# Kernel optimization log

Hardware: AMD Instinct MI355X
Metric: run time of the kernel (lower is better)

## Reference

```python
import jax, jax.numpy as jnp
import numpy as np

C = 512

def setup_inputs() -> dict:
    key = jax.random.key(0)
    ks = jax.random.split(key, 7)
    x = jax.random.normal(ks[0], (4, C, 64, 64), dtype=jnp.float32)
    s = 1.0 / np.sqrt(C)
    f_w = jax.random.normal(ks[1], (C // 2, C), dtype=jnp.float32) * s
    f_b = jax.random.normal(ks[2], (C // 2,), dtype=jnp.float32) * 0.01
    g_w = jax.random.normal(ks[3], (C // 2, C), dtype=jnp.float32) * s
    g_b = jax.random.normal(ks[4], (C // 2,), dtype=jnp.float32) * 0.01
    h_w = jax.random.normal(ks[5], (C, C), dtype=jnp.float32) * s
    h_b = jax.random.normal(ks[6], (C,), dtype=jnp.float32) * 0.01
    return {"x": x, "f_w": f_w, "f_b": f_b, "g_w": g_w, "g_b": g_b, "h_w": h_w, "h_b": h_b}

def reference(x, f_w, f_b, g_w, g_b, h_w, h_b):
    B, Cc, H, W = x.shape
    N = H * W
    xf = x.reshape(B, Cc, N)  # hw_flatten
    # 1x1 convs are channel GEMMs: [B,Cout,N]
    f = jnp.einsum('oc,bcn->bon', f_w, xf) + f_b[None, :, None]
    g = jnp.einsum('oc,bcn->bon', g_w, xf) + g_b[None, :, None]
    h = jnp.einsum('oc,bcn->bon', h_w, xf) + h_b[None, :, None]
    # energy[b,i,j] = sum_k f[b,k,i] * g[b,k,j]
    energy = jnp.einsum('bki,bkj->bij', f, g)
    attention = jax.nn.softmax(energy, axis=-1)
    # ret[b,c,i] = sum_j h[b,c,j] * attention[b,i,j]
    ret = jnp.einsum('bcj,bij->bci', h, attention)
    return ret.reshape(B, Cc, H, W)
```

## Files before the change

kernel.cpp:

```cpp
#include <hip/hip_runtime.h>


#define NPIX 4096
#define CIN  512

typedef _Float16 f16x4 __attribute__((ext_vector_type(4)));
typedef _Float16 f16x8 __attribute__((ext_vector_type(8)));
typedef float    f32x4 __attribute__((ext_vector_type(4)));
typedef float    f32x16 __attribute__((ext_vector_type(16)));

#define MFMA16(a, b, c) __builtin_amdgcn_mfma_f32_16x16x16f16(a, b, c, 0, 0, 0)
#define MFMA32(a, b, c) __builtin_amdgcn_mfma_f32_32x32x16_f16(a, b, c, 0, 0, 0)

__device__ __forceinline__ void gld_lds16(const void* g, void* l) {
    __builtin_amdgcn_global_load_lds(
        (const __attribute__((address_space(1))) unsigned int*)g,
        (__attribute__((address_space(3))) unsigned int*)l, 16, 0, 0);
}

__global__ __launch_bounds__(256) void proj_kernel(
    const float* __restrict__ x,
    const float* __restrict__ f_w, const float* __restrict__ f_b,
    const float* __restrict__ g_w, const float* __restrict__ g_b,
    const float* __restrict__ h_w, const float* __restrict__ h_b,
    _Float16* __restrict__ qw, _Float16* __restrict__ kw,
    _Float16* __restrict__ vw)
{
    const int b  = blockIdx.z;
    const int n0 = blockIdx.x * 64;
    const int o0 = blockIdx.y * 64;

    const float* wsrc; const float* bsrc;
    if (o0 < 256)      { wsrc = f_w + (size_t)o0 * CIN;         bsrc = f_b + o0; }
    else if (o0 < 512) { wsrc = g_w + (size_t)(o0 - 256) * CIN; bsrc = g_b + (o0 - 256); }
    else               { wsrc = h_w + (size_t)(o0 - 512) * CIN; bsrc = h_b + (o0 - 512); }

    __shared__ _Float16 Wt[64][40];
    __shared__ _Float16 Xt[64][40];

    const int t = threadIdx.x;
    const int lane = t & 63, wv = t >> 6;
    const int wm = wv >> 1, wn = wv & 1;
    const int gi = lane >> 4, li = lane & 15;

    f32x4 acc[2][2];
    #pragma unroll
    for (int i = 0; i < 2; ++i)
        #pragma unroll
        for (int j = 0; j < 2; ++j) acc[i][j] = f32x4{0.f, 0.f, 0.f, 0.f};

    for (int kk = 0; kk < CIN; kk += 32) {
        {
            const int r = t >> 2, c8 = (t & 3) * 8;
            const float* p = wsrc + (size_t)r * CIN + kk + c8;
            const float4 v0 = *(const float4*)p;
            const float4 v1 = *(const float4*)(p + 4);
            f16x8 w8;
            w8[0] = (_Float16)v0.x; w8[1] = (_Float16)v0.y;
            w8[2] = (_Float16)v0.z; w8[3] = (_Float16)v0.w;
            w8[4] = (_Float16)v1.x; w8[5] = (_Float16)v1.y;
            w8[6] = (_Float16)v1.z; w8[7] = (_Float16)v1.w;
            *(f16x8*)&Wt[r][c8] = w8;
        }
        {
            const int cb = (t >> 6) * 8;
            const int nl = t & 63;
            f16x8 xv;
            #pragma unroll
            for (int e = 0; e < 8; ++e)
                xv[e] = (_Float16)x[((size_t)b * CIN + kk + cb + e) * NPIX +
                                    n0 + nl];
            *(f16x8*)&Xt[nl][cb] = xv;
        }
        __syncthreads();
        #pragma unroll
        for (int kh = 0; kh < 2; ++kh) {
            const int ko = kh * 16 + gi * 4;
            f16x4 a0 = *(const f16x4*)&Wt[wm * 32 +      li][ko];
            f16x4 a1 = *(const f16x4*)&Wt[wm * 32 + 16 + li][ko];
            f16x4 b0 = *(const f16x4*)&Xt[wn * 32 +      li][ko];
            f16x4 b1 = *(const f16x4*)&Xt[wn * 32 + 16 + li][ko];
            acc[0][0] = MFMA16(a0, b0, acc[0][0]);
            acc[0][1] = MFMA16(a0, b1, acc[0][1]);
            acc[1][0] = MFMA16(a1, b0, acc[1][0]);
            acc[1][1] = MFMA16(a1, b1, acc[1][1]);
        }
        __syncthreads();
    }

    #pragma unroll
    for (int mf = 0; mf < 2; ++mf)
        #pragma unroll
        for (int nf = 0; nf < 2; ++nf) {
            const int obase = o0 + wm * 32 + mf * 16 + gi * 4;
            const int n     = n0 + wn * 32 + nf * 16 + li;
            const int brel  = wm * 32 + mf * 16 + gi * 4;
            float v[4];
            #pragma unroll
            for (int r = 0; r < 4; ++r) v[r] = acc[mf][nf][r] + bsrc[brel + r];
            if (o0 < 512) {
                _Float16* dst = (o0 < 256) ? qw : kw;
                const int kb  = (o0 < 256) ? obase : (obase - 256);
                f16x4 pk;
                pk[0] = (_Float16)v[0]; pk[1] = (_Float16)v[1];
                pk[2] = (_Float16)v[2]; pk[3] = (_Float16)v[3];
                *(f16x4*)&dst[((size_t)b * NPIX + n) * 256 + kb] = pk;
            } else {
                #pragma unroll
                for (int r = 0; r < 4; ++r)
                    vw[((size_t)b * CIN + (obase - 512 + r)) * NPIX + n] =
                        (_Float16)v[r];
            }
        }
}

__global__ __launch_bounds__(512, 2) void attn_kernel(
    const _Float16* __restrict__ qw, const _Float16* __restrict__ kw,
    const _Float16* __restrict__ vw,
    _Float16* __restrict__ opart, float* __restrict__ stats)
{
    const int bid = blockIdx.x;
    const int xcd = bid & 7;
    const int jh = xcd & 1, b = xcd >> 1;
    const int rb = bid >> 3;
    const int t = threadIdx.x, l = t & 63, wv = t >> 6;
    const int li = l & 31, g = l >> 5;
    const int ch = wv & 1, rg = wv >> 1;
    const int i_row = rb * 128 + rg * 32 + li;

    __shared__ char Kt[2][16384];
    __shared__ char Vt[2][512 * 72];
    __shared__ char Pt[2][4][64 * 48];

    f16x8 qf[16];
    if (ch == 0) {
        const _Float16* qb = qw + ((size_t)b * NPIX + i_row) * 256 + 8 * g;
        #pragma unroll
        for (int ks = 0; ks < 16; ++ks) qf[ks] = *(const f16x8*)(qb + ks * 16);
    }

    f32x16 oacc[8];
    #pragma unroll
    for (int i = 0; i < 8; ++i)
        #pragma unroll
        for (int e = 0; e < 16; ++e) oacc[i][e] = 0.f;
    float m_run = -__builtin_inff();
    float l_run = 0.f;

    f16x8 vreg[4];

    auto stageK = [&](int buf, int j0) {
        #pragma unroll
        for (int q = 0; q < 2; ++q) {
            const int slot = q * 512 + t;
            const int row  = slot >> 5;
            const int colb = (slot & 31) * 16;
            const char* src =
                (const char*)(kw + ((size_t)b * NPIX + j0 + row) * 256) +
                (colb ^ ((row & 31) << 4));
            gld_lds16(src, Kt[buf] + slot * 16);
        }
    };
    auto loadV = [&](int j0) {
        #pragma unroll
        for (int q = 0; q < 4; ++q) {
            const int c  = q * 128 + (t >> 2);
            const int jj = (t & 3) * 8;
            vreg[q] = *(const f16x8*)(vw + ((size_t)b * CIN + c) * NPIX + j0 + jj);
        }
    };
    auto writeV = [&](int buf) {
        #pragma unroll
        for (int q = 0; q < 4; ++q) {
            const int c = q * 128 + (t >> 2);
            char* d = Vt[buf] + c * 72 + (t & 3) * 16;
            *(f16x4*)d       = *(f16x4*)&vreg[q];
            *(f16x4*)(d + 8) = *((f16x4*)&vreg[q] + 1);
        }
    };

    const int jbase = jh * 2048;
    stageK(0, jbase);
    loadV(jbase);
    writeV(0);
    __syncthreads();

    for (int it = 0; it < 64; ++it) {
        const int cur = it & 1;
        if (it < 63) {
            stageK(cur ^ 1, jbase + (it + 1) * 32);
            loadV(jbase + (it + 1) * 32);
        }

        f16x8 pa0, pa1;
        if (ch == 0) {
            f32x16 s;
            #pragma unroll
            for (int e = 0; e < 16; ++e) s[e] = 0.f;
            {
                const char* kr = Kt[cur] + li * 512;
                const int sw = li << 4;
                __builtin_amdgcn_s_setprio(1);
                #pragma unroll
                for (int ks = 0; ks < 16; ++ks) {
                    f16x8 kf = *(const f16x8*)(kr + ((ks * 32 + 16 * g) ^ sw));
                    s = MFMA32(kf, qf[ks], s);
                }
                __builtin_amdgcn_s_setprio(0);
            }

            float tmax = s[0];
            #pragma unroll
            for (int e = 1; e < 16; ++e) tmax = fmaxf(tmax, s[e]);
            tmax = fmaxf(tmax, __shfl_xor(tmax, 32));
            float sc_my = 1.0f;
            if (!__all((int)(tmax - m_run <= 5.f))) {
                const float mnew = fmaxf(m_run, tmax);
                sc_my = __expf(m_run - mnew);
                #pragma unroll
                for (int ct = 0; ct < 8; ++ct)
                    #pragma unroll
                    for (int e = 0; e < 16; ++e) oacc[ct][e] *= sc_my;
                l_run *= sc_my;
                m_run = mnew;
            }
            float p[16];
            float rs = 0.f;
            #pragma unroll
            for (int e = 0; e < 16; ++e) { p[e] = __expf(s[e] - m_run); rs += p[e]; }
            rs += __shfl_xor(rs, 32);
            l_run += rs;

            #pragma unroll
            for (int e = 0; e < 8; ++e) {
                pa0[e] = (_Float16)p[e];
                pa1[e] = (_Float16)p[8 + e];
            }
            char* pd = Pt[cur][rg] + l * 48;
            *(f16x8*)pd        = pa0;
            *(f16x8*)(pd + 16) = pa1;
            *(float*)(pd + 32) = sc_my;
        }
        __syncthreads();

        if (ch == 1) {
            const char* ps = Pt[cur][rg] + l * 48;
            pa0 = *(const f16x8*)ps;
            pa1 = *(const f16x8*)(ps + 16);
            const float sc = *(const float*)(ps + 32);
            if (!__all((int)(sc == 1.0f))) {
                #pragma unroll
                for (int ct = 0; ct < 8; ++ct)
                    #pragma unroll
                    for (int e = 0; e < 16; ++e) oacc[ct][e] *= sc;
            }
        }

        __builtin_amdgcn_s_setprio(1);
        #pragma unroll
        for (int ct = 0; ct < 8; ++ct) {
            const int c = ch * 256 + ct * 32 + li;
            const char* vr = Vt[cur] + c * 72;
            f16x8 va;
            *(f16x4*)&va       = *(const f16x4*)(vr + 8 * g);
            *((f16x4*)&va + 1) = *(const f16x4*)(vr + 16 + 8 * g);
            oacc[ct] = MFMA32(va, pa0, oacc[ct]);
            f16x8 vc;
            *(f16x4*)&vc       = *(const f16x4*)(vr + 32 + 8 * g);
            *((f16x4*)&vc + 1) = *(const f16x4*)(vr + 48 + 8 * g);
            oacc[ct] = MFMA32(vc, pa1, oacc[ct]);
        }
        __builtin_amdgcn_s_setprio(0);

        if (it < 63) writeV(cur ^ 1);
    }

    const size_t ob = (size_t)(jh * 4 + b) * CIN * NPIX;
    #pragma unroll
    for (int ct = 0; ct < 8; ++ct)
        #pragma unroll
        for (int r = 0; r < 16; ++r) {
            const int c = ch * 256 + ct * 32 + (r & 3) + 8 * (r >> 2) + 4 * g;
            opart[ob + (size_t)c * NPIX + i_row] = (_Float16)oacc[ct][r];
        }
    if (ch == 0 && g == 0) {
        const size_t idx = ((size_t)(jh * 4 + b) * NPIX + i_row) * 2;
        stats[idx]     = m_run;
        stats[idx + 1] = l_run;
    }
}

__global__ __launch_bounds__(256) void combine_kernel(
    const _Float16* __restrict__ opart, const float* __restrict__ stats,
    float* __restrict__ out)
{
    const int b  = blockIdx.y;
    const int i0 = blockIdx.x * 64;
    const int t  = threadIdx.x;

    __shared__ float a0s[64], a1s[64];
    if (t < 64) {
        const int i = i0 + t;
        const size_t r0 = ((size_t)b * NPIX + i) * 2;
        const size_t r1 = ((size_t)(4 + b) * NPIX + i) * 2;
        const float m0 = stats[r0], l0 = stats[r0 + 1];
        const float m1 = stats[r1], l1 = stats[r1 + 1];
        const float M  = fmaxf(m0, m1);
        const float w0 = __expf(m0 - M), w1 = __expf(m1 - M);
        const float inv = 1.0f / (l0 * w0 + l1 * w1);
        a0s[t] = w0 * inv;
        a1s[t] = w1 * inv;
    }
    __syncthreads();

    const int ci = t >> 3;
    const int ii = (t & 7) * 8;
    #pragma unroll 4
    for (int pp = 0; pp < 16; ++pp) {
        const int c = pp * 32 + ci;
        const _Float16* p0 = opart + ((size_t)b * CIN + c) * NPIX + i0 + ii;
        const _Float16* p1 = opart + ((size_t)(4 + b) * CIN + c) * NPIX + i0 + ii;
        const f16x8 x0 = *(const f16x8*)p0;
        const f16x8 x1 = *(const f16x8*)p1;
        float* dst = out + ((size_t)b * CIN + c) * NPIX + i0 + ii;
        float4 o0, o1;
        o0.x = a0s[ii + 0] * (float)x0[0] + a1s[ii + 0] * (float)x1[0];
        o0.y = a0s[ii + 1] * (float)x0[1] + a1s[ii + 1] * (float)x1[1];
        o0.z = a0s[ii + 2] * (float)x0[2] + a1s[ii + 2] * (float)x1[2];
        o0.w = a0s[ii + 3] * (float)x0[3] + a1s[ii + 3] * (float)x1[3];
        o1.x = a0s[ii + 4] * (float)x0[4] + a1s[ii + 4] * (float)x1[4];
        o1.y = a0s[ii + 5] * (float)x0[5] + a1s[ii + 5] * (float)x1[5];
        o1.z = a0s[ii + 6] * (float)x0[6] + a1s[ii + 6] * (float)x1[6];
        o1.w = a0s[ii + 7] * (float)x0[7] + a1s[ii + 7] * (float)x1[7];
        *(float4*)dst       = o0;
        *(float4*)(dst + 4) = o1;
    }
}

extern "C" void kernel_launch(void* const* d_in, const int* in_sizes, int n_in,
                              void* d_out, int out_size, void* d_ws,
                              size_t ws_size, hipStream_t stream)
{
    const float* x   = (const float*)d_in[0];
    const float* f_w = (const float*)d_in[1];
    const float* f_b = (const float*)d_in[2];
    const float* g_w = (const float*)d_in[3];
    const float* g_b = (const float*)d_in[4];
    const float* h_w = (const float*)d_in[5];
    const float* h_b = (const float*)d_in[6];
    float* out = (float*)d_out;

    _Float16* qw = (_Float16*)d_ws;
    _Float16* kw = qw + (size_t)4 * NPIX * 256;
    _Float16* vw = kw + (size_t)4 * NPIX * 256;
    _Float16* op = vw + (size_t)4 * CIN * NPIX;
    float* stats = (float*)(op + (size_t)2 * 4 * CIN * NPIX);

    proj_kernel<<<dim3(64, 16, 4), 256, 0, stream>>>(
        x, f_w, f_b, g_w, g_b, h_w, h_b, qw, kw, vw);
    attn_kernel<<<dim3(256), 512, 0, stream>>>(qw, kw, vw, op, stats);
    combine_kernel<<<dim3(64, 4), 256, 0, stream>>>(op, stats, out);
}
```

Before: 235.8 us.

## Software-pipeline attention so QK of step s overlaps PV of step s-1

Restructures the attention main loop so the score-computing waves (ch==0) run QK^T and softmax for the current key tile, then apply the previous tile's P·V for their share of channels. The other waves meanwhile do P·V for the previous tile. This drops one of the two __syncthreads per iteration, so softmax no longer stalls the PV waves. Channel work is rebalanced 192/320 between the two wave groups to offset the QK cost, and V writes to LDS are moved to the loop start. The trade-off is more accumulator registers (10 tiles) on the PV waves, which may reduce occupancy, plus extra prologue and epilogue code.

```diff
diff --git a/kernel.cpp b/kernel.cpp
--- a/kernel.cpp
+++ b/kernel.cpp
@@ -16,6 +16,31 @@
     __builtin_amdgcn_global_load_lds(
         (const __attribute__((address_space(1))) unsigned int*)g,
         (__attribute__((address_space(3))) unsigned int*)l, 16, 0, 0);
+}
+
+template<int NCT, int CB>
+__device__ __forceinline__ void pv_step(f32x16* oacc, const char* vb,
+                                        int li, int g, f16x8 pa0, f16x8 pa1) {
+    #pragma unroll
+    for (int ct = 0; ct < NCT; ++ct) {
+        const int c = CB + ct * 32 + li;
+        const char* vr = vb + c * 72;
+        f16x8 va, vc;
+        *(f16x4*)&va       = *(const f16x4*)(vr + 8 * g);
+        *((f16x4*)&va + 1) = *(const f16x4*)(vr + 16 + 8 * g);
+        oacc[ct] = MFMA32(va, pa0, oacc[ct]);
+        *(f16x4*)&vc       = *(const f16x4*)(vr + 32 + 8 * g);
+        *((f16x4*)&vc + 1) = *(const f16x4*)(vr + 48 + 8 * g);
+        oacc[ct] = MFMA32(vc, pa1, oacc[ct]);
+    }
+}
+
+template<int N>
+__device__ __forceinline__ void rescale_acc(f32x16* o, float sc) {
+    #pragma unroll
+    for (int ct = 0; ct < N; ++ct)
+        #pragma unroll
+        for (int e = 0; e < 16; ++e) o[ct][e] *= sc;
 }
 
 __global__ __launch_bounds__(256) void proj_kernel(
@@ -125,7 +150,7 @@
     const int rb = bid >> 3;
     const int t = threadIdx.x, l = t & 63, wv = t >> 6;
     const int li = l & 31, g = l >> 5;
-    const int ch = wv & 1, rg = wv >> 1;
+    const int ch = wv >> 2, rg = wv & 3;
     const int i_row = rb * 128 + rg * 32 + li;
 
     __shared__ char Kt[2][16384];
@@ -139,15 +164,19 @@
         for (int ks = 0; ks < 16; ++ks) qf[ks] = *(const f16x8*)(qb + ks * 16);
     }
 
-    f32x16 oacc[8];
-    #pragma unroll
-    for (int i = 0; i < 8; ++i)
+    f32x16 oacc[10];
+    #pragma unroll
+    for (int i = 0; i < 10; ++i)
         #pragma unroll
         for (int e = 0; e < 16; ++e) oacc[i][e] = 0.f;
     float m_run = -__builtin_inff();
     float l_run = 0.f;
 
     f16x8 vreg[4];
+    f16x8 paA, paB;
+    float sc_prev = 1.0f;
+    #pragma unroll
+    for (int e = 0; e < 8; ++e) { paA[e] = (_Float16)0; paB[e] = (_Float16)0; }
 
     auto stageK = [&](int buf, int j0) {
         #pragma unroll
@@ -180,23 +209,28 @@
     };
 
     const int jbase = jh * 2048;
+    loadV(jbase);
     stageK(0, jbase);
-    loadV(jbase);
-    writeV(0);
+    if (ch == 0) {
+        char* pd = Pt[1][rg] + l * 48;
+        *(f16x8*)pd        = paA;
+        *(f16x8*)(pd + 16) = paB;
+        *(float*)(pd + 32) = 1.0f;
+    }
     __syncthreads();
 
-    for (int it = 0; it < 64; ++it) {
-        const int cur = it & 1;
-        if (it < 63) {
-            stageK(cur ^ 1, jbase + (it + 1) * 32);
-            loadV(jbase + (it + 1) * 32);
-        }
-
-        f16x8 pa0, pa1;
+    for (int s = 0; s < 64; ++s) {
+        const int cur = s & 1;
+        writeV(cur);
+        if (s < 63) {
+            stageK(cur ^ 1, jbase + (s + 1) * 32);
+            loadV(jbase + (s + 1) * 32);
+        }
+
         if (ch == 0) {
-            f32x16 s;
-            #pragma unroll
-            for (int e = 0; e < 16; ++e) s[e] = 0.f;
+            f32x16 sv;
+            #pragma unroll
+            for (int e = 0; e < 16; ++e) sv[e] = 0.f;
             {
                 const char* kr = Kt[cur] + li * 512;
                 const int sw = li << 4;
@@ -204,33 +238,30 @@
                 #pragma unroll
                 for (int ks = 0; ks < 16; ++ks) {
                     f16x8 kf = *(const f16x8*)(kr + ((ks * 32 + 16 * g) ^ sw));
-                    s = MFMA32(kf, qf[ks], s);
+                    sv = MFMA32(kf, qf[ks], sv);
                 }
                 __builtin_amdgcn_s_setprio(0);
             }
 
-            float tmax = s[0];
-            #pragma unroll
-            for (int e = 1; e < 16; ++e) tmax = fmaxf(tmax, s[e]);
+            float tmax = sv[0];
+            #pragma unroll
+            for (int e = 1; e < 16; ++e) tmax = fmaxf(tmax, sv[e]);
             tmax = fmaxf(tmax, __shfl_xor(tmax, 32));
-            float sc_my = 1.0f;
+            float sc_new = 1.0f;
             if (!__all((int)(tmax - m_run <= 5.f))) {
                 const float mnew = fmaxf(m_run, tmax);
-                sc_my = __expf(m_run - mnew);
-                #pragma unroll
-                for (int ct = 0; ct < 8; ++ct)
-                    #pragma unroll
-                    for (int e = 0; e < 16; ++e) oacc[ct][e] *= sc_my;
-                l_run *= sc_my;
+                sc_new = __expf(m_run - mnew);
+                l_run *= sc_new;
                 m_run = mnew;
             }
             float p[16];
             float rs = 0.f;
             #pragma unroll
-            for (int e = 0; e < 16; ++e) { p[e] = __expf(s[e] - m_run); rs += p[e]; }
+            for (int e = 0; e < 16; ++e) { p[e] = __expf(sv[e] - m_run); rs += p[e]; }
             rs += __shfl_xor(rs, 32);
             l_run += rs;
 
+            f16x8 pa0, pa1;
             #pragma unroll
             for (int e = 0; e < 8; ++e) {
                 pa0[e] = (_Float16)p[e];
@@ -239,54 +270,64 @@
             char* pd = Pt[cur][rg] + l * 48;
             *(f16x8*)pd        = pa0;
             *(f16x8*)(pd + 16) = pa1;
-            *(float*)(pd + 32) = sc_my;
+            *(float*)(pd + 32) = sc_new;
+
+            if (s > 0) {
+                if (!__all((int)(sc_prev == 1.f))) rescale_acc<6>(oacc, sc_prev);
+                __builtin_amdgcn_s_setprio(1);
+                pv_step<6, 0>(oacc, Vt[cur ^ 1], li, g, paA, paB);
+                __builtin_amdgcn_s_setprio(0);
+            }
+            paA = pa0; paB = pa1; sc_prev = sc_new;
+        } else {
+            if (s > 0) {
+                const char* ps = Pt[cur ^ 1][rg] + l * 48;
+                f16x8 pa0 = *(const f16x8*)ps;
+                f16x8 pa1 = *(const f16x8*)(ps + 16);
+                const float sc = *(const float*)(ps + 32);
+                if (!__all((int)(sc == 1.f))) rescale_acc<10>(oacc, sc);
+                __builtin_amdgcn_s_setprio(1);
+                pv_step<10, 192>(oacc, Vt[cur ^ 1], li, g, pa0, pa1);
+                __builtin_amdgcn_s_setprio(0);
+            }
         }
         __syncthreads();
-
-        if (ch == 1) {
-            const char* ps = Pt[cur][rg] + l * 48;
-            pa0 = *(const f16x8*)ps;
-            pa1 = *(const f16x8*)(ps + 16);
-            const float sc = *(const float*)(ps + 32);
-            if (!__all((int)(sc == 1.0f))) {
-                #pragma unroll
-                for (int ct = 0; ct < 8; ++ct)
-                    #pragma unroll
-                    for (int e = 0; e < 16; ++e) oacc[ct][e] *= sc;
-            }
-        }
-
-        __builtin_amdgcn_s_setprio(1);
-        #pragma unroll
-        for (int ct = 0; ct < 8; ++ct) {
-            const int c = ch * 256 + ct * 32 + li;
-            const char* vr = Vt[cur] + c * 72;
-            f16x8 va;
-            *(f16x4*)&va       = *(const f16x4*)(vr + 8 * g);
-            *((f16x4*)&va + 1) = *(const f16x4*)(vr + 16 + 8 * g);
-            oacc[ct] = MFMA32(va, pa0, oacc[ct]);
-            f16x8 vc;
-            *(f16x4*)&vc       = *(const f16x4*)(vr + 32 + 8 * g);
-            *((f16x4*)&vc + 1) = *(const f16x4*)(vr + 48 + 8 * g);
-            oacc[ct] = MFMA32(vc, pa1, oacc[ct]);
-        }
-        __builtin_amdgcn_s_setprio(0);
-
-        if (it < 63) writeV(cur ^ 1);
+    }
+
+    if (ch == 0) {
+        if (!__all((int)(sc_prev == 1.f))) rescale_acc<6>(oacc, sc_prev);
+        pv_step<6, 0>(oacc, Vt[1], li, g, paA, paB);
+    } else {
+        const char* ps = Pt[1][rg] + l * 48;
+        f16x8 pa0 = *(const f16x8*)ps;
+        f16x8 pa1 = *(const f16x8*)(ps + 16);
+        const float sc = *(const float*)(ps + 32);
+        if (!__all((int)(sc == 1.f))) rescale_acc<10>(oacc, sc);
+        pv_step<10, 192>(oacc, Vt[1], li, g, pa0, pa1);
     }
 
     const size_t ob = (size_t)(jh * 4 + b) * CIN * NPIX;
-    #pragma unroll
-    for (int ct = 0; ct < 8; ++ct)
-        #pragma unroll
-        for (int r = 0; r < 16; ++r) {
-            const int c = ch * 256 + ct * 32 + (r & 3) + 8 * (r >> 2) + 4 * g;
-            opart[ob + (size_t)c * NPIX + i_row] = (_Float16)oacc[ct][r];
-        }
-    if (ch == 0 && g == 0) {
-        const size_t idx = ((size_t)(jh * 4 + b) * NPIX + i_row) * 2;
-        stats[idx]     = m_run;
-        stats[idx + 1] = l_run;
+    if (ch == 0) {
+        #pragma unroll
+        for (int ct = 0; ct < 6; ++ct)
+            #pragma unroll
+            for (int r = 0; r < 16; ++r) {
+                const int c = ct * 32 + (r & 3) + 8 * (r >> 2) + 4 * g;
+                opart[ob + (size_t)c * NPIX + i_row] = (_Float16)oacc[ct][r];
+            }
+        if (g == 0) {
+            const size_t idx = ((size_t)(jh * 4 + b) * NPIX + i_row) * 2;
+            stats[idx]     = m_run;
+            stats[idx + 1] = l_run;
+        }
+    } else {
+        #pragma unroll
+        for (int ct = 0; ct < 10; ++ct)
+            #pragma unroll
+            for (int r = 0; r < 16; ++r) {
+                const int c = 192 + ct * 32 + (r & 3) + 8 * (r >> 2) + 4 * g;
+                opart[ob + (size_t)c * NPIX + i_row] = (_Float16)oacc[ct][r];
+            }
     }
 }
 
```

After: 457.2 us. 93.9% more time.

## Restructure attention loop synchronization with explicit waitcnts and split barriers

Applied to the files above, without the earlier changes.

The attention main loop now issues the next V register loads before the K stage, then waits on vmcnt explicitly so only the previous iteration's K tile has to have landed. It replaces __syncthreads with raw s_barrier calls plus manual lgkmcnt waits. The P exchange buffer becomes single-buffered, and the two wave roles get separate branches that each run their own PV MFMA loop after the barrier. The aim is to cut redundant full waits and give finer control over how memory traffic overlaps with MFMA work. In exchange, correctness now depends on hand-counted vmcnt values and barrier ordering, which is fragile.

```diff
diff --git a/kernel.cpp b/kernel.cpp
--- a/kernel.cpp
+++ b/kernel.cpp
@@ -130,7 +130,7 @@
 
     __shared__ char Kt[2][16384];
     __shared__ char Vt[2][512 * 72];
-    __shared__ char Pt[2][4][64 * 48];
+    __shared__ char Pt[4][64 * 48];
 
     f16x8 qf[16];
     if (ch == 0) {
@@ -180,23 +180,28 @@
     };
 
     const int jbase = jh * 2048;
+    loadV(jbase);
     stageK(0, jbase);
-    loadV(jbase);
     writeV(0);
     __syncthreads();
 
-    for (int it = 0; it < 64; ++it) {
-        const int cur = it & 1;
-        if (it < 63) {
-            stageK(cur ^ 1, jbase + (it + 1) * 32);
-            loadV(jbase + (it + 1) * 32);
-        }
-
-        f16x8 pa0, pa1;
+    for (int s = 0; s < 64; ++s) {
+        const int cur = s & 1;
+
+        if (s < 63) {
+            loadV(jbase + (s + 1) * 32);
+            stageK(cur ^ 1, jbase + (s + 1) * 32);
+            asm volatile("s_waitcnt vmcnt(6)" ::: "memory");
+        } else {
+            asm volatile("s_waitcnt vmcnt(0)" ::: "memory");
+        }
+        __builtin_amdgcn_sched_barrier(0);
+        __builtin_amdgcn_s_barrier();
+
         if (ch == 0) {
-            f32x16 s;
-            #pragma unroll
-            for (int e = 0; e < 16; ++e) s[e] = 0.f;
+            f32x16 sv;
+            #pragma unroll
+            for (int e = 0; e < 16; ++e) sv[e] = 0.f;
             {
                 const char* kr = Kt[cur] + li * 512;
                 const int sw = li << 4;
@@ -204,14 +209,14 @@
                 #pragma unroll
                 for (int ks = 0; ks < 16; ++ks) {
                     f16x8 kf = *(const f16x8*)(kr + ((ks * 32 + 16 * g) ^ sw));
-                    s = MFMA32(kf, qf[ks], s);
+                    sv = MFMA32(kf, qf[ks], sv);
                 }
                 __builtin_amdgcn_s_setprio(0);
             }
 
-            float tmax = s[0];
-            #pragma unroll
-            for (int e = 1; e < 16; ++e) tmax = fmaxf(tmax, s[e]);
+            float tmax = sv[0];
+            #pragma unroll
+            for (int e = 1; e < 16; ++e) tmax = fmaxf(tmax, sv[e]);
             tmax = fmaxf(tmax, __shfl_xor(tmax, 32));
             float sc_my = 1.0f;
             if (!__all((int)(tmax - m_run <= 5.f))) {
@@ -227,26 +232,45 @@
             float p[16];
             float rs = 0.f;
             #pragma unroll
-            for (int e = 0; e < 16; ++e) { p[e] = __expf(s[e] - m_run); rs += p[e]; }
+            for (int e = 0; e < 16; ++e) { p[e] = __expf(sv[e] - m_run); rs += p[e]; }
             rs += __shfl_xor(rs, 32);
             l_run += rs;
 
+            f16x8 pa0, pa1;
             #pragma unroll
             for (int e = 0; e < 8; ++e) {
                 pa0[e] = (_Float16)p[e];
                 pa1[e] = (_Float16)p[8 + e];
             }
-            char* pd = Pt[cur][rg] + l * 48;
+            char* pd = Pt[rg] + l * 48;
             *(f16x8*)pd        = pa0;
             *(f16x8*)(pd + 16) = pa1;
             *(float*)(pd + 32) = sc_my;
-        }
-        __syncthreads();
-
-        if (ch == 1) {
-            const char* ps = Pt[cur][rg] + l * 48;
-            pa0 = *(const f16x8*)ps;
-            pa1 = *(const f16x8*)(ps + 16);
+
+            asm volatile("s_waitcnt lgkmcnt(0)" ::: "memory");
+            __builtin_amdgcn_s_barrier();
+
+            __builtin_amdgcn_s_setprio(1);
+            #pragma unroll
+            for (int ct = 0; ct < 8; ++ct) {
+                const int c = ct * 32 + li;
+                const char* vr = Vt[cur] + c * 72;
+                f16x8 va, vc;
+                *(f16x4*)&va       = *(const f16x4*)(vr + 8 * g);
+                *((f16x4*)&va + 1) = *(const f16x4*)(vr + 16 + 8 * g);
+                oacc[ct] = MFMA32(va, pa0, oacc[ct]);
+                *(f16x4*)&vc       = *(const f16x4*)(vr + 32 + 8 * g);
+                *((f16x4*)&vc + 1) = *(const f16x4*)(vr + 48 + 8 * g);
+                oacc[ct] = MFMA32(vc, pa1, oacc[ct]);
+            }
+            __builtin_amdgcn_s_setprio(0);
+        } else {
+            asm volatile("s_waitcnt lgkmcnt(0)" ::: "memory");
+            __builtin_amdgcn_s_barrier();
+
+            const char* ps = Pt[rg] + l * 48;
+            f16x8 pa0 = *(const f16x8*)ps;
+            f16x8 pa1 = *(const f16x8*)(ps + 16);
             const float sc = *(const float*)(ps + 32);
             if (!__all((int)(sc == 1.0f))) {
                 #pragma unroll
@@ -254,25 +278,25 @@
                     #pragma unroll
                     for (int e = 0; e < 16; ++e) oacc[ct][e] *= sc;
             }
-        }
-
-        __builtin_amdgcn_s_setprio(1);
-        #pragma unroll
-        for (int ct = 0; ct < 8; ++ct) {
-            const int c = ch * 256 + ct * 32 + li;
-            const char* vr = Vt[cur] + c * 72;
-            f16x8 va;
-            *(f16x4*)&va       = *(const f16x4*)(vr + 8 * g);
-            *((f16x4*)&va + 1) = *(const f16x4*)(vr + 16 + 8 * g);
-            oacc[ct] = MFMA32(va, pa0, oacc[ct]);
-            f16x8 vc;
-            *(f16x4*)&vc       = *(const f16x4*)(vr + 32 + 8 * g);
-            *((f16x4*)&vc + 1) = *(const f16x4*)(vr + 48 + 8 * g);
-            oacc[ct] = MFMA32(vc, pa1, oacc[ct]);
-        }
-        __builtin_amdgcn_s_setprio(0);
-
-        if (it < 63) writeV(cur ^ 1);
+            __builtin_amdgcn_s_setprio(1);
+            #pragma unroll
+            for (int ct = 0; ct < 8; ++ct) {
+                const int c = 256 + ct * 32 + li;
+                const char* vr = Vt[cur] + c * 72;
+                f16x8 va, vc;
+                *(f16x4*)&va       = *(const f16x4*)(vr + 8 * g);
+                *((f16x4*)&va + 1) = *(const f16x4*)(vr + 16 + 8 * g);
+                oacc[ct] = MFMA32(va, pa0, oacc[ct]);
+                *(f16x4*)&vc       = *(const f16x4*)(vr + 32 + 8 * g);
+                *((f16x4*)&vc + 1) = *(const f16x4*)(vr + 48 + 8 * g);
+                oacc[ct] = MFMA32(vc, pa1, oacc[ct]);
+            }
+            __builtin_amdgcn_s_setprio(0);
+        }
+
+        if (s < 63) writeV(cur ^ 1);
+        asm volatile("s_waitcnt lgkmcnt(0)" ::: "memory");
+        __builtin_amdgcn_sched_barrier(0);
     }
 
     const size_t ob = (size_t)(jh * 4 + b) * CIN * NPIX;
```

Result: slower. 320.4 us (+35.9%).

## Split attention into one QK-softmax producer wave and four PV consumer waves

Applied to the files above, without the earlier changes.

Restructures the attention kernel into a warp-specialized pipeline. A single producer wave computes QK scores and softmax probabilities one step ahead into double-buffered shared memory. Four consumer waves each own 128 output channels and run the PV MFMAs while also prefetching K two steps ahead and V one step ahead. Each block now covers 32 query rows instead of 128, so the grid grows to 1024 blocks of 320 threads. The aim is to overlap softmax with PV and shorten each wave's accumulator set, at the cost of each block re-streaming K/V for fewer rows, which raises L2 and global traffic.

```diff
diff --git a/kernel.cpp b/kernel.cpp
--- a/kernel.cpp
+++ b/kernel.cpp
@@ -114,7 +114,7 @@
         }
 }
 
-__global__ __launch_bounds__(512, 2) void attn_kernel(
+__global__ __launch_bounds__(320, 3) void attn_kernel(
     const _Float16* __restrict__ qw, const _Float16* __restrict__ kw,
     const _Float16* __restrict__ vw,
     _Float16* __restrict__ opart, float* __restrict__ stats)
@@ -125,34 +125,37 @@
     const int rb = bid >> 3;
     const int t = threadIdx.x, l = t & 63, wv = t >> 6;
     const int li = l & 31, g = l >> 5;
-    const int ch = wv & 1, rg = wv >> 1;
-    const int i_row = rb * 128 + rg * 32 + li;
+    const int i_row = rb * 32 + li;
+    const bool prod = (wv == 4);
+    const int cw = wv;
 
     __shared__ char Kt[2][16384];
-    __shared__ char Vt[2][512 * 72];
-    __shared__ char Pt[2][4][64 * 48];
+    __shared__ char Vt[512 * 72];
+    __shared__ char PtA[2][64 * 16];
+    __shared__ char PtB[2][64 * 16];
+    __shared__ char PtS[2][64 * 4];
 
     f16x8 qf[16];
-    if (ch == 0) {
+    if (prod) {
         const _Float16* qb = qw + ((size_t)b * NPIX + i_row) * 256 + 8 * g;
         #pragma unroll
         for (int ks = 0; ks < 16; ++ks) qf[ks] = *(const f16x8*)(qb + ks * 16);
     }
 
-    f32x16 oacc[8];
+    f32x16 oacc[4];
     #pragma unroll
-    for (int i = 0; i < 8; ++i)
+    for (int i = 0; i < 4; ++i)
         #pragma unroll
         for (int e = 0; e < 16; ++e) oacc[i][e] = 0.f;
     float m_run = -__builtin_inff();
     float l_run = 0.f;
 
-    f16x8 vreg[4];
+    f16x8 vreg[8];
 
     auto stageK = [&](int buf, int j0) {
         #pragma unroll
-        for (int q = 0; q < 2; ++q) {
-            const int slot = q * 512 + t;
+        for (int q = 0; q < 4; ++q) {
+            const int slot = q * 256 + t;
             const int row  = slot >> 5;
             const int colb = (slot & 31) * 16;
             const char* src =
@@ -163,127 +166,130 @@
     };
     auto loadV = [&](int j0) {
         #pragma unroll
-        for (int q = 0; q < 4; ++q) {
-            const int c  = q * 128 + (t >> 2);
-            const int jj = (t & 3) * 8;
-            vreg[q] = *(const f16x8*)(vw + ((size_t)b * CIN + c) * NPIX + j0 + jj);
+        for (int q = 0; q < 8; ++q) {
+            const int c = cw * 128 + q * 16 + (l >> 2);
+            vreg[q] = *(const f16x8*)(vw + ((size_t)b * CIN + c) * NPIX + j0 +
+                                      (l & 3) * 8);
         }
     };
-    auto writeV = [&](int buf) {
-        #pragma unroll
-        for (int q = 0; q < 4; ++q) {
-            const int c = q * 128 + (t >> 2);
-            char* d = Vt[buf] + c * 72 + (t & 3) * 16;
+    auto writeV = [&]() {
+        #pragma unroll
+        for (int q = 0; q < 8; ++q) {
+            const int c = cw * 128 + q * 16 + (l >> 2);
+            char* d = Vt + c * 72 + (l & 3) * 16;
             *(f16x4*)d       = *(f16x4*)&vreg[q];
             *(f16x4*)(d + 8) = *((f16x4*)&vreg[q] + 1);
         }
     };
 
+    auto produce = [&](int kbuf, int pbuf) {
+        f32x16 sa, sb;
+        #pragma unroll
+        for (int e = 0; e < 16; ++e) { sa[e] = 0.f; sb[e] = 0.f; }
+        const char* kr = Kt[kbuf] + li * 512;
+        const int sw = li << 4;
+        __builtin_amdgcn_s_setprio(1);
+        #pragma unroll
+        for (int ks = 0; ks < 8; ++ks) {
+            f16x8 k0 = *(const f16x8*)(kr + ((ks * 32 + 16 * g) ^ sw));
+            f16x8 k1 = *(const f16x8*)(kr + (((ks + 8) * 32 + 16 * g) ^ sw));
+            sa = MFMA32(k0, qf[ks], sa);
+            sb = MFMA32(k1, qf[ks + 8], sb);
+        }
+        __builtin_amdgcn_s_setprio(0);
+        f32x16 sv;
+        #pragma unroll
+        for (int e = 0; e < 16; ++e) sv[e] = sa[e] + sb[e];
+
+        float m0 = fmaxf(fmaxf(sv[0], sv[1]), fmaxf(sv[2], sv[3]));
+        float m1 = fmaxf(fmaxf(sv[4], sv[5]), fmaxf(sv[6], sv[7]));
+        float m2 = fmaxf(fmaxf(sv[8], sv[9]), fmaxf(sv[10], sv[11]));
+        float m3 = fmaxf(fmaxf(sv[12], sv[13]), fmaxf(sv[14], sv[15]));
+        float tmax = fmaxf(fmaxf(m0, m1), fmaxf(m2, m3));
+        tmax = fmaxf(tmax, __shfl_xor(tmax, 32));
+        float sc_my = 1.0f;
+        if (!__all((int)(tmax - m_run <= 5.f))) {
+            const float mnew = fmaxf(m_run, tmax);
+            sc_my = __expf(m_run - mnew);
+            l_run *= sc_my;
+            m_run = mnew;
+        }
+        float p[16];
+        float rs = 0.f;
+        #pragma unroll
+        for (int e = 0; e < 16; ++e) { p[e] = __expf(sv[e] - m_run); rs += p[e]; }
+        rs += __shfl_xor(rs, 32);
+        l_run += rs;
+
+        f16x8 pa0, pa1;
+        #pragma unroll
+        for (int e = 0; e < 8; ++e) {
+            pa0[e] = (_Float16)p[e];
+            pa1[e] = (_Float16)p[8 + e];
+        }
+        *(f16x8*)(PtA[pbuf] + l * 16) = pa0;
+        *(f16x8*)(PtB[pbuf] + l * 16) = pa1;
+        *(float*)(PtS[pbuf] + l * 4)  = sc_my;
+    };
+
     const int jbase = jh * 2048;
-    stageK(0, jbase);
-    loadV(jbase);
-    writeV(0);
+
+    if (!prod) {
+        stageK(0, jbase);
+        stageK(1, jbase + 32);
+        loadV(jbase);
+    }
     __syncthreads();
-
-    for (int it = 0; it < 64; ++it) {
-        const int cur = it & 1;
-        if (it < 63) {
-            stageK(cur ^ 1, jbase + (it + 1) * 32);
-            loadV(jbase + (it + 1) * 32);
-        }
-
-        f16x8 pa0, pa1;
-        if (ch == 0) {
-            f32x16 s;
-            #pragma unroll
-            for (int e = 0; e < 16; ++e) s[e] = 0.f;
-            {
-                const char* kr = Kt[cur] + li * 512;
-                const int sw = li << 4;
-                __builtin_amdgcn_s_setprio(1);
-                #pragma unroll
-                for (int ks = 0; ks < 16; ++ks) {
-                    f16x8 kf = *(const f16x8*)(kr + ((ks * 32 + 16 * g) ^ sw));
-                    s = MFMA32(kf, qf[ks], s);
-                }
-                __builtin_amdgcn_s_setprio(0);
-            }
-
-            float tmax = s[0];
-            #pragma unroll
-            for (int e = 1; e < 16; ++e) tmax = fmaxf(tmax, s[e]);
-            tmax = fmaxf(tmax, __shfl_xor(tmax, 32));
-            float sc_my = 1.0f;
-            if (!__all((int)(tmax - m_run <= 5.f))) {
-                const float mnew = fmaxf(m_run, tmax);
-                sc_my = __expf(m_run - mnew);
-                #pragma unroll
-                for (int ct = 0; ct < 8; ++ct)
-                    #pragma unroll
-                    for (int e = 0; e < 16; ++e) oacc[ct][e] *= sc_my;
-                l_run *= sc_my;
-                m_run = mnew;
-            }
-            float p[16];
-            float rs = 0.f;
-            #pragma unroll
-            for (int e = 0; e < 16; ++e) { p[e] = __expf(s[e] - m_run); rs += p[e]; }
-            rs += __shfl_xor(rs, 32);
-            l_run += rs;
-
-            #pragma unroll
-            for (int e = 0; e < 8; ++e) {
-                pa0[e] = (_Float16)p[e];
-                pa1[e] = (_Float16)p[8 + e];
-            }
-            char* pd = Pt[cur][rg] + l * 48;
-            *(f16x8*)pd        = pa0;
-            *(f16x8*)(pd + 16) = pa1;
-            *(float*)(pd + 32) = sc_my;
-        }
-        __syncthreads();
-
-        if (ch == 1) {
-            const char* ps = Pt[cur][rg] + l * 48;
-            pa0 = *(const f16x8*)ps;
-            pa1 = *(const f16x8*)(ps + 16);
-            const float sc = *(const float*)(ps + 32);
+    if (prod) produce(0, 0);
+    else      writeV();
+    __syncthreads();
+
+    for (int s = 0; s < 64; ++s) {
+        if (prod) {
+            if (s < 63) produce((s + 1) & 1, (s + 1) & 1);
+        } else {
+            if (s < 62) stageK(s & 1, jbase + (s + 2) * 32);
+            if (s < 63) loadV(jbase + (s + 1) * 32);
+
+            f16x8 pa0 = *(const f16x8*)(PtA[s & 1] + l * 16);
+            f16x8 pa1 = *(const f16x8*)(PtB[s & 1] + l * 16);
+            const float sc = *(const float*)(PtS[s & 1] + l * 4);
             if (!__all((int)(sc == 1.0f))) {
                 #pragma unroll
-                for (int ct = 0; ct < 8; ++ct)
+                for (int ct = 0; ct < 4; ++ct)
                     #pragma unroll
                     for (int e = 0; e < 16; ++e) oacc[ct][e] *= sc;
             }
-        }
-
-        __builtin_amdgcn_s_setprio(1);
-        #pragma unroll
-        for (int ct = 0; ct < 8; ++ct) {
-            const int c = ch * 256 + ct * 32 + li;
-            const char* vr = Vt[cur] + c * 72;
-            f16x8 va;
-            *(f16x4*)&va       = *(const f16x4*)(vr + 8 * g);
-            *((f16x4*)&va + 1) = *(const f16x4*)(vr + 16 + 8 * g);
-            oacc[ct] = MFMA32(va, pa0, oacc[ct]);
-            f16x8 vc;
-            *(f16x4*)&vc       = *(const f16x4*)(vr + 32 + 8 * g);
-            *((f16x4*)&vc + 1) = *(const f16x4*)(vr + 48 + 8 * g);
-            oacc[ct] = MFMA32(vc, pa1, oacc[ct]);
-        }
-        __builtin_amdgcn_s_setprio(0);
-
-        if (it < 63) writeV(cur ^ 1);
-    }
-
-    const size_t ob = (size_t)(jh * 4 + b) * CIN * NPIX;
-    #pragma unroll
-    for (int ct = 0; ct < 8; ++ct)
-        #pragma unroll
-        for (int r = 0; r < 16; ++r) {
-            const int c = ch * 256 + ct * 32 + (r & 3) + 8 * (r >> 2) + 4 * g;
-            opart[ob + (size_t)c * NPIX + i_row] = (_Float16)oacc[ct][r];
-        }
-    if (ch == 0 && g == 0) {
+            __builtin_amdgcn_s_setprio(1);
+            #pragma unroll
+            for (int ct = 0; ct < 4; ++ct) {
+                const int c = cw * 128 + ct * 32 + li;
+                const char* vr = Vt + c * 72;
+                f16x8 va, vc;
+                *(f16x4*)&va       = *(const f16x4*)(vr + 8 * g);
+                *((f16x4*)&va + 1) = *(const f16x4*)(vr + 16 + 8 * g);
+                oacc[ct] = MFMA32(va, pa0, oacc[ct]);
+                *(f16x4*)&vc       = *(const f16x4*)(vr + 32 + 8 * g);
+                *((f16x4*)&vc + 1) = *(const f16x4*)(vr + 48 + 8 * g);
+                oacc[ct] = MFMA32(vc, pa1, oacc[ct]);
+            }
+            __builtin_amdgcn_s_setprio(0);
+
+            if (s < 63) writeV();
+        }
+        __syncthreads();
+    }
+
+    if (!prod) {
+        const size_t ob = (size_t)(jh * 4 + b) * CIN * NPIX;
+        #pragma unroll
+        for (int ct = 0; ct < 4; ++ct)
+            #pragma unroll
+            for (int r = 0; r < 16; ++r) {
+                const int c = cw * 128 + ct * 32 + (r & 3) + 8 * (r >> 2) + 4 * g;
+                opart[ob + (size_t)c * NPIX + i_row] = (_Float16)oacc[ct][r];
+            }
+    } else if (g == 0) {
         const size_t idx = ((size_t)(jh * 4 + b) * NPIX + i_row) * 2;
         stats[idx]     = m_run;
         stats[idx + 1] = l_run;
@@ -358,6 +364,6 @@
 
     proj_kernel<<<dim3(64, 16, 4), 256, 0, stream>>>(
         x, f_w, f_b, g_w, g_b, h_w, h_b, qw, kw, vw);
-    attn_kernel<<<dim3(256), 512, 0, stream>>>(qw, kw, vw, op, stats);
+    attn_kernel<<<dim3(1024), 320, 0, stream>>>(qw, kw, vw, op, stats);
     combine_kernel<<<dim3(64, 4), 256, 0, stream>>>(op, stats, out);
 }
```

New measurement: 713.4 us. +202.5%, slower.
